# Performance work log

Measured on AMD Instinct MI355X. Metric: run time of the kernel, lower is better.

## Reference

```python
import jax, jax.numpy as jnp
import numpy as np

N = 27          # n_agents
NA = 33         # n_actions
OFF = 6         # semantic_action_offset
ATK = NA - OFF  # 27 attack actions
HID = 256       # rnn_hidden_dim
HEADS = 4
HD = 16         # head_dim
V = 8           # comm_value_dim
REL = 5
TOPK = 4
IN = 322
FLAT = HEADS * V  # 32
FUSE_SCALE = 0.1
GATE_FLOOR = 0.0
NEG = -1e10


def setup_inputs() -> dict:
    key = jax.random.key(0)
    ks = iter(jax.random.split(key, 40))
    r = lambda *s: jax.random.normal(next(ks), s, dtype=jnp.float32) * 0.05
    BS = 1024
    inp = {
        'inputs': jax.random.normal(next(ks), (BS * N, IN), dtype=jnp.float32),
        'hidden_state': jax.random.normal(next(ks), (BS * N, HID), dtype=jnp.float32),
        'relation_features': jax.random.normal(next(ks), (BS, N, N, REL), dtype=jnp.float32),
        'W1': r(HID, IN), 'b1': r(HID),
        'Wih': r(3 * HID, HID), 'bih': r(3 * HID),
        'Whh': r(3 * HID, HID), 'bhh': r(3 * HID),
        'Wp1': r(HID, HID), 'bp1': r(HID),
        'Wp2': r(NA, HID), 'bp2': r(NA),
        'Wq': r(HEADS * HD, HID), 'bq': r(HEADS * HD),
        'Wk': r(HEADS * HD, HID + REL), 'bk': r(HEADS * HD),
        'Wv': r(HEADS * V, ATK + 2), 'bv': r(HEADS * V),
        'ln_g': jnp.ones((FLAT,), jnp.float32), 'ln_b': jnp.zeros((FLAT,), jnp.float32),
        'Wg1': r(HID, HID + FLAT), 'bg1': r(HID),
        'Wg2': r(1, HID), 'bg2': jnp.full((1,), -2.5, jnp.float32),  # attack_gate_init_bias
        'Wd1': r(HID, HID + FLAT), 'bd1': r(HID),
        'Wd2': r(ATK, HID) * 0.2, 'bd2': r(ATK) * 0.2,  # small random instead of zero-init for nontrivial test
        'null_key': r(HEADS, HD), 'null_value': r(HEADS, V),
        'bs': BS,
    }
    return inp


def _topk_mask(scores, k):
    # scores: [bs, N, N+1, HEADS]; keep top-k along axis 2
    st = jnp.moveaxis(scores, 2, -1)                # [bs, N, HEADS, N+1]
    thr = jax.lax.top_k(st, k)[0][..., -1:]
    st = jnp.where(st >= thr, st, NEG)
    return jnp.moveaxis(st, -1, 2)


def _forward(inputs, hidden_state, relation_features, W1, b1, Wih, bih, Whh, bhh,
             Wp1, bp1, Wp2, bp2, Wq, bq, Wk, bk, Wv, bv, ln_g, ln_b,
             Wg1, bg1, Wg2, bg2, Wd1, bd1, Wd2, bd2, null_key, null_value, bs):
    x = jax.nn.relu(inputs @ W1.T + b1)
    h_in = hidden_state.reshape(-1, HID)
    # PyTorch GRUCell
    gi = x @ Wih.T + bih
    gh = h_in @ Whh.T + bhh
    ir, iz, inn = jnp.split(gi, 3, axis=-1)
    hr, hz, hn = jnp.split(gh, 3, axis=-1)
    rg = jax.nn.sigmoid(ir + hr)
    zg = jax.nn.sigmoid(iz + hz)
    ng = jnp.tanh(inn + rg * hn)
    h = (1.0 - zg) * ng + zg * h_in

    ah = h.reshape(bs, N, HID)                       # agent_hidden
    logits = jax.nn.relu(ah @ Wp1.T + bp1) @ Wp2.T + bp2   # [bs,N,NA]
    base_logits = logits[:, :, :OFF]
    attack_logits = logits[:, :, OFF:]

    # intent features (avail_actions=None path)
    attack_probs = jax.nn.softmax(attack_logits, axis=-1)
    top1 = jnp.max(attack_probs, axis=-1, keepdims=True)
    can_attack = jnp.ones((bs, N, 1), attack_probs.dtype)
    value_source = jnp.concatenate([attack_probs, can_attack, top1], axis=-1)
    sender_values = (value_source @ Wv.T + bv).reshape(bs, N, HEADS, V)

    queries = (ah @ Wq.T + bq).reshape(bs, N, HEADS, HD)
    # Linear over concat([sender_hidden, relation]) == split-weight sum
    Wk_h, Wk_r = Wk[:, :HID], Wk[:, HID:]
    key_h = ah @ Wk_h.T                              # [bs, N(send), A]
    key_r = jnp.einsum('bijr,ar->bija', relation_features, Wk_r)
    pair_keys = (key_h[:, None, :, :] + key_r + bk).reshape(bs, N, N, HEADS, HD)

    scale = 1.0 / np.sqrt(HD)
    scores = jnp.einsum('bihd,bijhd->bijh', queries, pair_keys) * scale
    eye = jnp.eye(N, dtype=bool)[None, :, :, None]
    scores = jnp.where(eye, NEG, scores)
    null_scores = jnp.einsum('bihd,hd->bih', queries, null_key)[:, :, None, :] * scale
    scores = jnp.concatenate([scores, null_scores], axis=2)   # [bs,N,N+1,HEADS]

    alpha = jax.nn.softmax(_topk_mask(scores, TOPK), axis=2)
    messages = (jnp.einsum('bijh,bjhv->bihv', alpha[:, :, :N], sender_values)
                + alpha[:, :, N, :, None] * null_value)        # [bs,N,HEADS,V]
    flat = messages.reshape(bs, N, FLAT)
    mu = jnp.mean(flat, axis=-1, keepdims=True)
    var = jnp.var(flat, axis=-1, keepdims=True)
    normed = (flat - mu) * jax.lax.rsqrt(var + 1e-5) * ln_g + ln_b

    fusion = jnp.concatenate([ah, normed], axis=-1)
    raw_gate = jax.nn.sigmoid(jax.nn.relu(fusion @ Wg1.T + bg1) @ Wg2.T + bg2)
    gate = GATE_FLOOR + (1.0 - GATE_FLOOR) * raw_gate
    delta = jax.nn.relu(fusion @ Wd1.T + bd1) @ Wd2.T + bd2
    fused = attack_logits + FUSE_SCALE * gate * delta
    final = jnp.concatenate([base_logits, fused], axis=-1).reshape(bs * N, NA)
    return final, h


def reference(inputs, hidden_state, relation_features, W1, b1, Wih, bih, Whh, bhh,
              Wp1, bp1, Wp2, bp2, Wq, bq, Wk, bk, Wv, bv, ln_g, ln_b,
              Wg1, bg1, Wg2, bg2, Wd1, bd1, Wd2, bd2, null_key, null_value, bs):
    return _forward(inputs, hidden_state, relation_features, W1, b1, Wih, bih, Whh, bhh,
                    Wp1, bp1, Wp2, bp2, Wq, bq, Wk, bk, Wv, bv, ln_g, ln_b,
                    Wg1, bg1, Wg2, bg2, Wd1, bd1, Wd2, bd2, null_key, null_value, bs)
```

## Files before the change

### kernel.cpp

```cpp
#include <hip/hip_runtime.h>
#include <cstdint>
#include <cstddef>

#define ROWS 27648
#define NEGV (-1e10f)

typedef __attribute__((ext_vector_type(8))) short bf16x8;
typedef __attribute__((ext_vector_type(4))) short short4v;
typedef __attribute__((ext_vector_type(4))) float f32x4;

__device__ __forceinline__ float sigmoidf_(float x) { return 1.f / (1.f + __expf(-x)); }
__device__ __forceinline__ float bf2f(short s) {
  union { float f; unsigned u; } x; x.u = ((unsigned)(unsigned short)s) << 16; return x.f;
}
__device__ __forceinline__ short f2bf(float f) {
  union { float f; unsigned u; } x; x.f = f;
  unsigned r = (x.u + 0x7fffu + ((x.u >> 16) & 1u)) >> 16;
  return (short)r;
}

#define GLDS(gp, lp) __builtin_amdgcn_global_load_lds( \
  (const __attribute__((address_space(1))) void*)(gp), \
  (__attribute__((address_space(3))) void*)(lp), 16, 0, 0)

template <int ACT, int BF16OUT>
__global__ __launch_bounds__(256) void gemm_mfma(
    const short* __restrict__ A, int lda,
    const short* __restrict__ B, int ldb,
    const float* __restrict__ bias,
    void* __restrict__ Cv, int ldc, int nstore, int K) {
  __shared__ short As[128 * 32];
  __shared__ short Bs[128 * 32];
  const int tid = threadIdx.x;
  const int wave = tid >> 6, lane = tid & 63;
  const int m0 = blockIdx.y * 128, n0 = blockIdx.x * 128;
  const int srow = lane >> 2, scol = (lane & 3) * 8;
  const int sr0 = wave * 32;
  const int wm = (wave >> 1) * 64, wn = (wave & 1) * 64;
  const int fr = lane & 15, fk = (lane >> 4) * 8;

  f32x4 acc[4][4] = {};

  const short* pA0 = A + (size_t)(m0 + sr0 + srow) * lda + scol;
  const short* pA1 = pA0 + 16 * lda;
  const short* pB0 = B + (size_t)(n0 + sr0 + srow) * ldb + scol;
  const short* pB1 = pB0 + 16 * ldb;
  short* lA0 = &As[sr0 * 32];
  short* lA1 = &As[(sr0 + 16) * 32];
  short* lB0 = &Bs[sr0 * 32];
  short* lB1 = &Bs[(sr0 + 16) * 32];

  for (int k0 = 0; k0 < K; k0 += 32) {
    GLDS(pA0 + k0, lA0);
    GLDS(pA1 + k0, lA1);
    GLDS(pB0 + k0, lB0);
    GLDS(pB1 + k0, lB1);
    __syncthreads();
    bf16x8 af[4], bfr[4];
#pragma unroll
    for (int t = 0; t < 4; ++t) {
      af[t]  = *(const bf16x8*)&As[(wm + t * 16 + fr) * 32 + fk];
      bfr[t] = *(const bf16x8*)&Bs[(wn + t * 16 + fr) * 32 + fk];
    }
#pragma unroll
    for (int i = 0; i < 4; ++i)
#pragma unroll
      for (int j = 0; j < 4; ++j)
        acc[i][j] = __builtin_amdgcn_mfma_f32_16x16x32_bf16(af[i], bfr[j], acc[i][j], 0, 0, 0);
    __syncthreads();
  }

  const int rbase = m0 + wm + (lane >> 4) * 4;
#pragma unroll
  for (int j = 0; j < 4; ++j) {
    const int col = n0 + wn + j * 16 + fr;
    if (col >= nstore) continue;
    const float bv = bias ? bias[col] : 0.f;
#pragma unroll
    for (int i = 0; i < 4; ++i)
#pragma unroll
      for (int r = 0; r < 4; ++r) {
        const int row = rbase + i * 16 + r;
        float v = acc[i][j][r] + bv;
        if (ACT) v = fmaxf(v, 0.f);
        if (BF16OUT) ((short*)Cv)[(size_t)row * ldc + col] = f2bf(v);
        else         ((float*)Cv)[(size_t)row * ldc + col] = v;
      }
  }
}

__global__ __launch_bounds__(256) void gemm_pqk(
    const short* __restrict__ A, const short* __restrict__ B,
    const float* __restrict__ bias,
    short* __restrict__ P1, float* __restrict__ QK) {
  __shared__ short As[128 * 32];
  __shared__ short Bs[128 * 32];
  const int tid = threadIdx.x;
  const int wave = tid >> 6, lane = tid & 63;
  const int m0 = blockIdx.y * 128, n0 = blockIdx.x * 128;
  const int srow = lane >> 2, scol = (lane & 3) * 8;
  const int sr0 = wave * 32;
  const int wm = (wave >> 1) * 64, wn = (wave & 1) * 64;
  const int fr = lane & 15, fk = (lane >> 4) * 8;

  f32x4 acc[4][4] = {};
  const short* pA0 = A + (size_t)(m0 + sr0 + srow) * 288 + scol;
  const short* pA1 = pA0 + 16 * 288;
  const short* pB0 = B + (size_t)(n0 + sr0 + srow) * 256 + scol;
  const short* pB1 = pB0 + 16 * 256;
  short* lA0 = &As[sr0 * 32];
  short* lA1 = &As[(sr0 + 16) * 32];
  short* lB0 = &Bs[sr0 * 32];
  short* lB1 = &Bs[(sr0 + 16) * 32];

  for (int k0 = 0; k0 < 256; k0 += 32) {
    GLDS(pA0 + k0, lA0);
    GLDS(pA1 + k0, lA1);
    GLDS(pB0 + k0, lB0);
    GLDS(pB1 + k0, lB1);
    __syncthreads();
    bf16x8 af[4], bfr[4];
#pragma unroll
    for (int t = 0; t < 4; ++t) {
      af[t]  = *(const bf16x8*)&As[(wm + t * 16 + fr) * 32 + fk];
      bfr[t] = *(const bf16x8*)&Bs[(wn + t * 16 + fr) * 32 + fk];
    }
#pragma unroll
    for (int i = 0; i < 4; ++i)
#pragma unroll
      for (int j = 0; j < 4; ++j)
        acc[i][j] = __builtin_amdgcn_mfma_f32_16x16x32_bf16(af[i], bfr[j], acc[i][j], 0, 0, 0);
    __syncthreads();
  }

  const int rbase = m0 + wm + (lane >> 4) * 4;
#pragma unroll
  for (int j = 0; j < 4; ++j) {
    const int col = n0 + wn + j * 16 + fr;
    if (col >= 384) continue;
    const float bv = bias[col];
#pragma unroll
    for (int i = 0; i < 4; ++i)
#pragma unroll
      for (int r = 0; r < 4; ++r) {
        const int row = rbase + i * 16 + r;
        float v = acc[i][j][r] + bv;
        if (col < 256) {
          P1[(size_t)row * 256 + col] = f2bf(fmaxf(v, 0.f));
        } else {
          QK[(size_t)row * 128 + (col - 256)] = v;
        }
      }
  }
}

__global__ __launch_bounds__(256) void conv_acts(
    const float* __restrict__ inputs, const float* __restrict__ hidden,
    short* __restrict__ xin, short* __restrict__ hid) {
  const int NX = ROWS * 352;
  int idx = blockIdx.x * 256 + threadIdx.x;
  if (idx < NX) {
    int row = idx / 352, c = idx - row * 352;
    xin[idx] = (c < 322) ? f2bf(inputs[row * 322 + c]) : (short)0;
  } else {
    int j = idx - NX;
    if (j < ROWS * 256) hid[j] = f2bf(hidden[j]);
  }
}

__global__ __launch_bounds__(256) void conv_w(
    const float* __restrict__ W1, const float* __restrict__ Wih,
    const float* __restrict__ Whh, const float* __restrict__ Wp1,
    const float* __restrict__ Wp2, const float* __restrict__ Wq,
    const float* __restrict__ Wk, const float* __restrict__ Wg1,
    const float* __restrict__ Wd1, const float* __restrict__ Wg2,
    const float* __restrict__ Wd2, const float* __restrict__ bp1,
    const float* __restrict__ bq, const float* __restrict__ bg1,
    const float* __restrict__ bd1, const float* __restrict__ bg2,
    const float* __restrict__ bd2,
    short* __restrict__ w1w, short* __restrict__ wihw, short* __restrict__ whhw,
    short* __restrict__ wp2w, short* __restrict__ wpqk, short* __restrict__ wgdw,
    short* __restrict__ wfw, float* __restrict__ bpqkb, float* __restrict__ bgd,
    float* __restrict__ bf2v) {
  int idx = blockIdx.x * 256 + threadIdx.x;
  if (idx < 90112) {
    int r = idx / 352, c = idx - r * 352;
    w1w[idx] = (c < 322) ? f2bf(W1[r * 322 + c]) : (short)0;
    return;
  }
  idx -= 90112;
  if (idx < 196608) { wihw[idx] = f2bf(Wih[idx]); return; }
  idx -= 196608;
  if (idx < 196608) { whhw[idx] = f2bf(Whh[idx]); return; }
  idx -= 196608;
  if (idx < 32768) {
    wp2w[idx] = (idx < 33 * 256) ? f2bf(Wp2[idx]) : (short)0;
    return;
  }
  idx -= 32768;
  if (idx < 131072) {
    int r = idx >> 8, c = idx & 255;
    short v = 0;
    if (r < 256) v = f2bf(Wp1[r * 256 + c]);
    else if (r < 320) v = f2bf(Wq[(r - 256) * 256 + c]);
    else if (r < 384) v = f2bf(Wk[(size_t)(r - 320) * 261 + c]);
    wpqk[idx] = v;
    return;
  }
  idx -= 131072;
  if (idx < 147456) {
    wgdw[idx] = (idx < 73728) ? f2bf(Wg1[idx]) : f2bf(Wd1[idx - 73728]);
    return;
  }
  idx -= 147456;
  if (idx < 65536) {
    int r = idx >> 9, c = idx & 511;
    short v = 0;
    if (r == 0 && c < 256) v = f2bf(Wg2[c]);
    else if (r >= 1 && r < 28 && c >= 256) v = f2bf(Wd2[(r - 1) * 256 + (c - 256)]);
    wfw[idx] = v;
    return;
  }
  idx -= 65536;
  if (idx < 384) {
    bpqkb[idx] = (idx < 256) ? bp1[idx] : ((idx < 320) ? bq[idx - 256] : 0.f);
    return;
  }
  idx -= 384;
  if (idx < 512) { bgd[idx] = (idx < 256) ? bg1[idx] : bd1[idx - 256]; return; }
  idx -= 512;
  if (idx < 128)
    bf2v[idx] = (idx == 0) ? bg2[0] : ((idx < 28) ? bd2[idx - 1] : 0.f);
}

__global__ __launch_bounds__(256) void gru_kernel(
    const short* __restrict__ GI, const short* __restrict__ GH,
    const float* __restrict__ Hin, float* __restrict__ H,
    short* __restrict__ FUS) {
  int idx = blockIdx.x * 256 + threadIdx.x;
  int row = idx >> 6;
  int c = (idx & 63) * 4;
  const short4v gr = *(const short4v*)(GI + (size_t)row * 768 + c);
  const short4v gz = *(const short4v*)(GI + (size_t)row * 768 + 256 + c);
  const short4v gn = *(const short4v*)(GI + (size_t)row * 768 + 512 + c);
  const short4v hr = *(const short4v*)(GH + (size_t)row * 768 + c);
  const short4v hz = *(const short4v*)(GH + (size_t)row * 768 + 256 + c);
  const short4v hn = *(const short4v*)(GH + (size_t)row * 768 + 512 + c);
  const f32x4 hi = *(const f32x4*)(Hin + (size_t)row * 256 + c);
  f32x4 o;
  short4v ob;
#pragma unroll
  for (int p = 0; p < 4; ++p) {
    float r = sigmoidf_(bf2f(gr[p]) + bf2f(hr[p]));
    float z = sigmoidf_(bf2f(gz[p]) + bf2f(hz[p]));
    float n = tanhf(bf2f(gn[p]) + r * bf2f(hn[p]));
    float h = (1.f - z) * n + z * hi[p];
    o[p] = h;
    ob[p] = f2bf(h);
  }
  *(f32x4*)(H + (size_t)row * 256 + c) = o;
  *(short4v*)(FUS + (size_t)row * 288 + c) = ob;
}

__global__ __launch_bounds__(256) void attn_sv_kernel(
    const float* __restrict__ QK, const float* __restrict__ rel,
    const float* __restrict__ Wk, const float* __restrict__ bk,
    const float* __restrict__ LOG, const float* __restrict__ Wv,
    const float* __restrict__ bv, const float* __restrict__ null_key,
    const float* __restrict__ null_value, const float* __restrict__ ln_g,
    const float* __restrict__ ln_b, short* __restrict__ FUS) {
  const int b = blockIdx.x;
  const int t = threadIdx.x;
  __shared__ float qk_s[27 * 129];
  __shared__ float rel_s[3645];
  __shared__ float lg_s[729];
  __shared__ float vs_s[27 * 29];
  __shared__ float sv_s[27 * 32];
  __shared__ float wv_s[32 * 29];
  __shared__ float wkr_s[320];
  __shared__ float bk_s[64], nk_s[64];
  __shared__ float nv_s[32], bv_s[32], lng_s[32], lnb_s[32];
  __shared__ float s_s[27 * 113];
  __shared__ float m_s[27 * 32];
  __shared__ float mu_s[27], rs_s[27];

  for (int idx = t; idx < 27 * 128; idx += 256) {
    int r = idx >> 7, c = idx & 127;
    qk_s[r * 129 + c] = QK[(size_t)(b * 27 + r) * 128 + c];
  }
  for (int idx = t; idx < 3645; idx += 256) rel_s[idx] = rel[(size_t)b * 3645 + idx];
  for (int idx = t; idx < 729; idx += 256) {
    int i = idx / 27, j = idx - i * 27;
    lg_s[idx] = LOG[(size_t)(b * 27 + i) * 33 + 6 + j];
  }
  for (int idx = t; idx < 32 * 29; idx += 256) wv_s[idx] = Wv[idx];
  if (t < 320) { int a = t / 5, r = t - a * 5; wkr_s[t] = Wk[(size_t)a * 261 + 256 + r]; }
  if (t < 64) { bk_s[t] = bk[t]; nk_s[t] = null_key[t]; }
  if (t < 32) { nv_s[t] = null_value[t]; bv_s[t] = bv[t]; lng_s[t] = ln_g[t]; lnb_s[t] = ln_b[t]; }
  __syncthreads();

  if (t < 27) {
    float m = -INFINITY;
    for (int j = 0; j < 27; ++j) m = fmaxf(m, lg_s[t * 27 + j]);
    float s = 0.f;
    for (int j = 0; j < 27; ++j) { float e = __expf(lg_s[t * 27 + j] - m); vs_s[t * 29 + j] = e; s += e; }
    float inv = 1.f / s;
    for (int j = 0; j < 27; ++j) vs_s[t * 29 + j] *= inv;
    vs_s[t * 29 + 27] = 1.f;
    vs_s[t * 29 + 28] = inv;
  }
  __syncthreads();

  for (int idx = t; idx < 864; idx += 256) {
    int j = idx >> 5, o = idx & 31;
    float acc = bv_s[o];
    const float* w = &wv_s[o * 29];
    const float* v = &vs_s[j * 29];
#pragma unroll
    for (int c = 0; c < 29; ++c) acc += w[c] * v[c];
    sv_s[idx] = acc;
  }
  for (int idx = t; idx < 3024; idx += 256) {
    int i = idx / 112, r2 = idx - i * 112;
    int j = r2 >> 2, h = r2 & 3;
    float s;
    if (j < 27) {
      const float* rp = &rel_s[(i * 27 + j) * 5];
      float r0 = rp[0], r1 = rp[1], rc = rp[2], r3 = rp[3], r4 = rp[4];
      const float* q = &qk_s[i * 129];
      const float* kh = &qk_s[j * 129 + 64 + h * 16];
      s = 0.f;
#pragma unroll
      for (int d = 0; d < 16; ++d) {
        int a = h * 16 + d;
        float kr = wkr_s[a * 5] * r0 + wkr_s[a * 5 + 1] * r1 + wkr_s[a * 5 + 2] * rc +
                   wkr_s[a * 5 + 3] * r3 + wkr_s[a * 5 + 4] * r4;
        s += q[a] * (kh[d] + kr + bk_s[a]);
      }
      s *= 0.25f;
      if (j == i) s = NEGV;
    } else {
      const float* q = &qk_s[i * 129 + h * 16];
      s = 0.f;
#pragma unroll
      for (int d = 0; d < 16; ++d) s += q[d] * nk_s[h * 16 + d];
      s *= 0.25f;
    }
    s_s[i * 113 + r2] = s;
  }
  __syncthreads();

  for (int idx = t; idx < 108; idx += 256) {
    int i = idx >> 2, h = idx & 3;
    float* sp = &s_s[i * 113 + h];
    float t0 = -INFINITY, t1 = -INFINITY, t2 = -INFINITY, t3 = -INFINITY;
    for (int j = 0; j < 28; ++j) {
      float v = sp[j * 4];
      if (v > t0)      { t3 = t2; t2 = t1; t1 = t0; t0 = v; }
      else if (v > t1) { t3 = t2; t2 = t1; t1 = v; }
      else if (v > t2) { t3 = t2; t2 = v; }
      else if (v > t3) { t3 = v; }
    }
    float sum = 0.f;
    for (int j = 0; j < 28; ++j) {
      float v = sp[j * 4];
      float e = (v >= t3) ? __expf(v - t0) : 0.f;
      sp[j * 4] = e; sum += e;
    }
    float inv = 1.f / sum;
    for (int j = 0; j < 28; ++j) sp[j * 4] *= inv;
  }
  __syncthreads();

  for (int idx = t; idx < 864; idx += 256) {
    int i = idx >> 5, o = idx & 31, h = o >> 3;
    const float* al = &s_s[i * 113 + h];
    float acc = al[27 * 4] * nv_s[o];
    for (int j = 0; j < 27; ++j) acc += al[j * 4] * sv_s[j * 32 + o];
    m_s[idx] = acc;
  }
  __syncthreads();

  if (t < 27) {
    float mu = 0.f;
    for (int k = 0; k < 32; ++k) mu += m_s[t * 32 + k];
    mu *= (1.f / 32.f);
    float var = 0.f;
    for (int k = 0; k < 32; ++k) { float d = m_s[t * 32 + k] - mu; var += d * d; }
    var *= (1.f / 32.f);
    mu_s[t] = mu; rs_s[t] = rsqrtf(var + 1e-5f);
  }
  __syncthreads();
  for (int idx = t; idx < 864; idx += 256) {
    int i = idx >> 5, o = idx & 31;
    float nv = (m_s[idx] - mu_s[i]) * rs_s[i] * lng_s[o] + lnb_s[o];
    FUS[(size_t)(b * 27 + i) * 288 + 256 + o] = f2bf(nv);
  }
}

__global__ __launch_bounds__(256) void fuse_kernel(
    const float* __restrict__ GDf, const float* __restrict__ LOG,
    float* __restrict__ out) {
  int idx = blockIdx.x * 256 + threadIdx.x;
  int row = idx / 33, c = idx - row * 33;
  float v = LOG[idx];
  if (c >= 6) {
    float gate = sigmoidf_(GDf[(size_t)row * 28]);
    v += 0.1f * gate * GDf[(size_t)row * 28 + (c - 5)];
  }
  out[idx] = v;
}

extern "C" void kernel_launch(void* const* d_in, const int* in_sizes, int n_in,
                              void* d_out, int out_size, void* d_ws, size_t ws_size,
                              hipStream_t stream) {
  const float* inputs = (const float*)d_in[0];
  const float* hidden = (const float*)d_in[1];
  const float* rel    = (const float*)d_in[2];
  const float* W1  = (const float*)d_in[3];  const float* b1  = (const float*)d_in[4];
  const float* Wih = (const float*)d_in[5];  const float* bih = (const float*)d_in[6];
  const float* Whh = (const float*)d_in[7];  const float* bhh = (const float*)d_in[8];
  const float* Wp1 = (const float*)d_in[9];  const float* bp1 = (const float*)d_in[10];
  const float* Wp2 = (const float*)d_in[11]; const float* bp2 = (const float*)d_in[12];
  const float* Wq  = (const float*)d_in[13]; const float* bq  = (const float*)d_in[14];
  const float* Wk  = (const float*)d_in[15]; const float* bk  = (const float*)d_in[16];
  const float* Wv  = (const float*)d_in[17]; const float* bv  = (const float*)d_in[18];
  const float* ln_g = (const float*)d_in[19]; const float* ln_b = (const float*)d_in[20];
  const float* Wg1 = (const float*)d_in[21]; const float* bg1 = (const float*)d_in[22];
  const float* Wg2 = (const float*)d_in[23]; const float* bg2 = (const float*)d_in[24];
  const float* Wd1 = (const float*)d_in[25]; const float* bd1 = (const float*)d_in[26];
  const float* Wd2 = (const float*)d_in[27]; const float* bd2 = (const float*)d_in[28];
  const float* null_key   = (const float*)d_in[29];
  const float* null_value = (const float*)d_in[30];

  char* wsb = (char*)d_ws;
  short* GIB = (short*)(wsb + 0);
  short* GDB = (short*)(wsb + 0);
  short* XINB = (short*)(wsb + 42467328);
  short* GHB  = (short*)(wsb + 42467328);
  float* LOG  = (float*)(wsb + 42467328);
  float* QKB  = (float*)(wsb + 42467328 + 4194304);
  float* LOGD = (float*)(wsb + 42467328 + 20971520);
  short* XB   = (short*)(wsb + 84934656);
  short* FUS  = (short*)(wsb + 84934656);
  short* HIDB = (short*)(wsb + 84934656 + 16777216);
  short* P1B  = (short*)(wsb + 84934656 + 16777216);
  char* wb = wsb + 115867648;
  short* W1W   = (short*)(wb + 0);
  short* WIHW  = (short*)(wb + 180224);
  short* WHHW  = (short*)(wb + 573440);
  short* WP2W  = (short*)(wb + 966656);
  short* WPQK  = (short*)(wb + 1032192);
  short* WGDW  = (short*)(wb + 1294336);
  short* WFW   = (short*)(wb + 1589248);
  float* BPQKb = (float*)(wb + 1720320);
  float* BGD   = (float*)(wb + 1721856);
  float* BF2   = (float*)(wb + 1723904);

  float* out = (float*)d_out;
  float* H   = out + (size_t)ROWS * 33;

  conv_acts<<<65664, 256, 0, stream>>>(inputs, hidden, XINB, HIDB);
  conv_w<<<3364, 256, 0, stream>>>(W1, Wih, Whh, Wp1, Wp2, Wq, Wk, Wg1, Wd1,
                                   Wg2, Wd2, bp1, bq, bg1, bd1, bg2, bd2,
                                   W1W, WIHW, WHHW, WP2W, WPQK, WGDW, WFW,
                                   BPQKb, BGD, BF2);
  gemm_mfma<1, 1><<<dim3(2, 216), 256, 0, stream>>>(XINB, 352, W1W, 352, b1, XB, 256, 256, 352);
  gemm_mfma<0, 1><<<dim3(6, 216), 256, 0, stream>>>(XB, 256, WIHW, 256, bih, GIB, 768, 768, 256);
  gemm_mfma<0, 1><<<dim3(6, 216), 256, 0, stream>>>(HIDB, 256, WHHW, 256, bhh, GHB, 768, 768, 256);
  gru_kernel<<<6912, 256, 0, stream>>>(GIB, GHB, hidden, H, FUS);
  gemm_pqk<<<dim3(3, 216), 256, 0, stream>>>(FUS, WPQK, BPQKb, P1B, QKB);
  gemm_mfma<0, 0><<<dim3(1, 216), 256, 0, stream>>>(P1B, 256, WP2W, 256, bp2, LOG, 33, 33, 256);
  attn_sv_kernel<<<1024, 256, 0, stream>>>(QKB, rel, Wk, bk, LOG, Wv, bv,
                                           null_key, null_value, ln_g, ln_b, FUS);
  gemm_mfma<1, 1><<<dim3(4, 216), 256, 0, stream>>>(FUS, 288, WGDW, 288, BGD, GDB, 512, 512, 288);
  gemm_mfma<0, 0><<<dim3(1, 216), 256, 0, stream>>>(GDB, 512, WFW, 512, BF2, LOGD, 28, 28, 512);
  fuse_kernel<<<3564, 256, 0, stream>>>(LOGD, LOG, out);
}
```

Baseline: 446.8 us.

## Split attention into per-row SV kernel and per-query-wave attention kernel

Replaces the single per-batch attention kernel, one block of 256 threads per batch, with two kernels. The first computes the softmaxed value projection (SV) per agent row, using wave shuffles for the reductions. The second assigns one wave per query agent across 7168 blocks. It precomputes q·Wk_rel, q·bk and q·null_key per head so the relation-key term becomes a 5-term dot product, and does the layer norm with shuffles instead of shared memory and extra barriers. The aim is more parallelism and fewer serial single-thread loops, at the cost of reloading K, SV and weights once per 4-query block and an extra global round trip for SV.

Result: no change. 445.0 us (-0.4%).

```diff
diff --git a/kernel.cpp b/kernel.cpp
--- a/kernel.cpp
+++ b/kernel.cpp
@@ -262,97 +262,123 @@
   *(short4v*)(FUS + (size_t)row * 288 + c) = ob;
 }
 
-__global__ __launch_bounds__(256) void attn_sv_kernel(
+__global__ __launch_bounds__(256) void sv_kernel(
+    const float* __restrict__ logits, const float* __restrict__ Wv,
+    const float* __restrict__ bv, float* __restrict__ SV) {
+  const int wave = threadIdx.x >> 6;
+  const int lane = threadIdx.x & 63;
+  const int row = blockIdx.x * 4 + wave;
+  __shared__ float vs_s[4][29];
+  float v = (lane < 27) ? logits[(size_t)row * 33 + 6 + lane] : -INFINITY;
+  float m = v;
+#pragma unroll
+  for (int off = 32; off; off >>= 1) m = fmaxf(m, __shfl_xor(m, off));
+  float e = (lane < 27) ? __expf(v - m) : 0.f;
+  float s = e;
+#pragma unroll
+  for (int off = 32; off; off >>= 1) s += __shfl_xor(s, off);
+  if (lane < 27) vs_s[wave][lane] = e / s;
+  if (lane == 27) vs_s[wave][27] = 1.f;
+  if (lane == 28) vs_s[wave][28] = 1.f / s;
+  __syncthreads();
+  if (lane < 32) {
+    float acc = bv[lane];
+    const float* w = Wv + lane * 29;
+#pragma unroll
+    for (int c = 0; c < 29; ++c) acc += w[c] * vs_s[wave][c];
+    SV[(size_t)row * 32 + lane] = acc;
+  }
+}
+
+__global__ __launch_bounds__(256) void attn2_kernel(
     const float* __restrict__ QK, const float* __restrict__ rel,
     const float* __restrict__ Wk, const float* __restrict__ bk,
-    const float* __restrict__ LOG, const float* __restrict__ Wv,
-    const float* __restrict__ bv, const float* __restrict__ null_key,
+    const float* __restrict__ SV, const float* __restrict__ null_key,
     const float* __restrict__ null_value, const float* __restrict__ ln_g,
     const float* __restrict__ ln_b, short* __restrict__ FUS) {
-  const int b = blockIdx.x;
+  const int b  = blockIdx.x / 7;
+  const int iq = blockIdx.x - b * 7;
   const int t = threadIdx.x;
-  __shared__ float qk_s[27 * 129];
-  __shared__ float rel_s[3645];
-  __shared__ float lg_s[729];
-  __shared__ float vs_s[27 * 29];
+  const int wave = t >> 6, lane = t & 63;
+  const int i = iq * 4 + wave;
+  const int iw = (i < 27) ? i : 26;
+
+  __shared__ float kh_s[27 * 64];
   __shared__ float sv_s[27 * 32];
-  __shared__ float wv_s[32 * 29];
+  __shared__ float q_s[4][64];
   __shared__ float wkr_s[320];
   __shared__ float bk_s[64], nk_s[64];
-  __shared__ float nv_s[32], bv_s[32], lng_s[32], lnb_s[32];
-  __shared__ float s_s[27 * 113];
-  __shared__ float m_s[27 * 32];
-  __shared__ float mu_s[27], rs_s[27];
-
-  for (int idx = t; idx < 27 * 128; idx += 256) {
-    int r = idx >> 7, c = idx & 127;
-    qk_s[r * 129 + c] = QK[(size_t)(b * 27 + r) * 128 + c];
-  }
-  for (int idx = t; idx < 3645; idx += 256) rel_s[idx] = rel[(size_t)b * 3645 + idx];
-  for (int idx = t; idx < 729; idx += 256) {
-    int i = idx / 27, j = idx - i * 27;
-    lg_s[idx] = LOG[(size_t)(b * 27 + i) * 33 + 6 + j];
-  }
-  for (int idx = t; idx < 32 * 29; idx += 256) wv_s[idx] = Wv[idx];
+  __shared__ float nv_s[32], lng_s[32], lnb_s[32];
+  __shared__ float rel_s[4][136];
+  __shared__ float qws[4][28];
+  __shared__ float s_row[4][112];
+
+  for (int idx = t; idx < 27 * 64; idx += 256) {
+    int r = idx >> 6, c = idx & 63;
+    kh_s[idx] = QK[(size_t)(b * 27 + r) * 128 + 64 + c];
+  }
+  for (int idx = t; idx < 27 * 32; idx += 256)
+    sv_s[idx] = SV[(size_t)b * 864 + idx];
+  q_s[wave][lane] = QK[(size_t)(b * 27 + iw) * 128 + lane];
   if (t < 320) { int a = t / 5, r = t - a * 5; wkr_s[t] = Wk[(size_t)a * 261 + 256 + r]; }
-  if (t < 64) { bk_s[t] = bk[t]; nk_s[t] = null_key[t]; }
-  if (t < 32) { nv_s[t] = null_value[t]; bv_s[t] = bv[t]; lng_s[t] = ln_g[t]; lnb_s[t] = ln_b[t]; }
+  if (t >= 320 && t < 384) bk_s[t - 320] = bk[t - 320];
+  if (t >= 384 && t < 448) nk_s[t - 384] = null_key[t - 384];
+  if (t >= 448 && t < 480) nv_s[t - 448] = null_value[t - 448];
+  if (t >= 480 && t < 512) { lng_s[t - 480] = ln_g[t - 480]; lnb_s[t - 480] = ln_b[t - 480]; }
+  for (int idx = lane; idx < 135; idx += 64)
+    rel_s[wave][idx] = rel[(size_t)(b * 27 + iw) * 135 + idx];
   __syncthreads();
 
-  if (t < 27) {
-    float m = -INFINITY;
-    for (int j = 0; j < 27; ++j) m = fmaxf(m, lg_s[t * 27 + j]);
-    float s = 0.f;
-    for (int j = 0; j < 27; ++j) { float e = __expf(lg_s[t * 27 + j] - m); vs_s[t * 29 + j] = e; s += e; }
-    float inv = 1.f / s;
-    for (int j = 0; j < 27; ++j) vs_s[t * 29 + j] *= inv;
-    vs_s[t * 29 + 27] = 1.f;
-    vs_s[t * 29 + 28] = inv;
+  if (lane < 28) {
+    float acc = 0.f;
+    if (lane < 20) {
+      const int h = lane / 5, r = lane - h * 5;
+#pragma unroll
+      for (int d = 0; d < 16; ++d)
+        acc += q_s[wave][h * 16 + d] * wkr_s[(h * 16 + d) * 5 + r];
+    } else if (lane < 24) {
+      const int h = lane - 20;
+#pragma unroll
+      for (int d = 0; d < 16; ++d)
+        acc += q_s[wave][h * 16 + d] * bk_s[h * 16 + d];
+    } else {
+      const int h = lane - 24;
+#pragma unroll
+      for (int d = 0; d < 16; ++d)
+        acc += q_s[wave][h * 16 + d] * nk_s[h * 16 + d];
+    }
+    qws[wave][lane] = acc;
   }
   __syncthreads();
 
-  for (int idx = t; idx < 864; idx += 256) {
-    int j = idx >> 5, o = idx & 31;
-    float acc = bv_s[o];
-    const float* w = &wv_s[o * 29];
-    const float* v = &vs_s[j * 29];
-#pragma unroll
-    for (int c = 0; c < 29; ++c) acc += w[c] * v[c];
-    sv_s[idx] = acc;
-  }
-  for (int idx = t; idx < 3024; idx += 256) {
-    int i = idx / 112, r2 = idx - i * 112;
-    int j = r2 >> 2, h = r2 & 3;
-    float s;
-    if (j < 27) {
-      const float* rp = &rel_s[(i * 27 + j) * 5];
-      float r0 = rp[0], r1 = rp[1], rc = rp[2], r3 = rp[3], r4 = rp[4];
-      const float* q = &qk_s[i * 129];
-      const float* kh = &qk_s[j * 129 + 64 + h * 16];
-      s = 0.f;
-#pragma unroll
-      for (int d = 0; d < 16; ++d) {
-        int a = h * 16 + d;
-        float kr = wkr_s[a * 5] * r0 + wkr_s[a * 5 + 1] * r1 + wkr_s[a * 5 + 2] * rc +
-                   wkr_s[a * 5 + 3] * r3 + wkr_s[a * 5 + 4] * r4;
-        s += q[a] * (kh[d] + kr + bk_s[a]);
+#pragma unroll
+  for (int pass = 0; pass < 2; ++pass) {
+    const int item = pass * 64 + lane;
+    if (item < 112) {
+      const int j = item >> 2, h = item & 3;
+      float s;
+      if (j < 27) {
+        float acc = qws[wave][20 + h];
+        const float* q  = &q_s[wave][h * 16];
+        const float* kh = &kh_s[j * 64 + h * 16];
+#pragma unroll
+        for (int d = 0; d < 16; ++d) acc += q[d] * kh[d];
+        const float* rp = &rel_s[wave][j * 5];
+        const float* qw = &qws[wave][h * 5];
+#pragma unroll
+        for (int r = 0; r < 5; ++r) acc += rp[r] * qw[r];
+        s = acc * 0.25f;
+        if (j == i) s = NEGV;
+      } else {
+        s = qws[wave][24 + h] * 0.25f;
       }
-      s *= 0.25f;
-      if (j == i) s = NEGV;
-    } else {
-      const float* q = &qk_s[i * 129 + h * 16];
-      s = 0.f;
-#pragma unroll
-      for (int d = 0; d < 16; ++d) s += q[d] * nk_s[h * 16 + d];
-      s *= 0.25f;
+      s_row[wave][item] = s;
     }
-    s_s[i * 113 + r2] = s;
   }
   __syncthreads();
 
-  for (int idx = t; idx < 108; idx += 256) {
-    int i = idx >> 2, h = idx & 3;
-    float* sp = &s_s[i * 113 + h];
+  if (lane < 4) {
+    float* sp = &s_row[wave][lane];
     float t0 = -INFINITY, t1 = -INFINITY, t2 = -INFINITY, t3 = -INFINITY;
     for (int j = 0; j < 28; ++j) {
       float v = sp[j * 4];
@@ -367,34 +393,28 @@
       float e = (v >= t3) ? __expf(v - t0) : 0.f;
       sp[j * 4] = e; sum += e;
     }
-    float inv = 1.f / sum;
+    const float inv = 1.f / sum;
     for (int j = 0; j < 28; ++j) sp[j * 4] *= inv;
   }
   __syncthreads();
 
-  for (int idx = t; idx < 864; idx += 256) {
-    int i = idx >> 5, o = idx & 31, h = o >> 3;
-    const float* al = &s_s[i * 113 + h];
-    float acc = al[27 * 4] * nv_s[o];
-    for (int j = 0; j < 27; ++j) acc += al[j * 4] * sv_s[j * 32 + o];
-    m_s[idx] = acc;
-  }
-  __syncthreads();
-
-  if (t < 27) {
-    float mu = 0.f;
-    for (int k = 0; k < 32; ++k) mu += m_s[t * 32 + k];
-    mu *= (1.f / 32.f);
-    float var = 0.f;
-    for (int k = 0; k < 32; ++k) { float d = m_s[t * 32 + k] - mu; var += d * d; }
-    var *= (1.f / 32.f);
-    mu_s[t] = mu; rs_s[t] = rsqrtf(var + 1e-5f);
-  }
-  __syncthreads();
-  for (int idx = t; idx < 864; idx += 256) {
-    int i = idx >> 5, o = idx & 31;
-    float nv = (m_s[idx] - mu_s[i]) * rs_s[i] * lng_s[o] + lnb_s[o];
-    FUS[(size_t)(b * 27 + i) * 288 + 256 + o] = f2bf(nv);
+  if (lane < 32) {
+    const int h = lane >> 3;
+    const float* al = &s_row[wave][h];
+    float acc = al[27 * 4] * nv_s[lane];
+    for (int j = 0; j < 27; ++j) acc += al[j * 4] * sv_s[j * 32 + lane];
+    float sum = acc;
+#pragma unroll
+    for (int off = 16; off; off >>= 1) sum += __shfl_xor(sum, off);
+    const float mu = sum * (1.f / 32.f);
+    float d = acc - mu;
+    float sq = d * d;
+#pragma unroll
+    for (int off = 16; off; off >>= 1) sq += __shfl_xor(sq, off);
+    const float rs = rsqrtf(sq * (1.f / 32.f) + 1e-5f);
+    const float nv = d * rs * lng_s[lane] + lnb_s[lane];
+    if (i < 27)
+      FUS[(size_t)(b * 27 + i) * 288 + 256 + lane] = f2bf(nv);
   }
 }
 
@@ -440,6 +460,7 @@
   short* GHB  = (short*)(wsb + 42467328);
   float* LOG  = (float*)(wsb + 42467328);
   float* QKB  = (float*)(wsb + 42467328 + 4194304);
+  float* SVB  = (float*)(wsb + 42467328 + 16777216);
   float* LOGD = (float*)(wsb + 42467328 + 20971520);
   short* XB   = (short*)(wsb + 84934656);
   short* FUS  = (short*)(wsb + 84934656);
@@ -471,8 +492,9 @@
   gru_kernel<<<6912, 256, 0, stream>>>(GIB, GHB, hidden, H, FUS);
   gemm_pqk<<<dim3(3, 216), 256, 0, stream>>>(FUS, WPQK, BPQKb, P1B, QKB);
   gemm_mfma<0, 0><<<dim3(1, 216), 256, 0, stream>>>(P1B, 256, WP2W, 256, bp2, LOG, 33, 33, 256);
-  attn_sv_kernel<<<1024, 256, 0, stream>>>(QKB, rel, Wk, bk, LOG, Wv, bv,
-                                           null_key, null_value, ln_g, ln_b, FUS);
+  sv_kernel<<<6912, 256, 0, stream>>>(LOG, Wv, bv, SVB);
+  attn2_kernel<<<7168, 256, 0, stream>>>(QKB, rel, Wk, bk, SVB, null_key,
+                                         null_value, ln_g, ln_b, FUS);
   gemm_mfma<1, 1><<<dim3(4, 216), 256, 0, stream>>>(FUS, 288, WGDW, 288, BGD, GDB, 512, 512, 288);
   gemm_mfma<0, 0><<<dim3(1, 216), 256, 0, stream>>>(GDB, 512, WFW, 512, BF2, LOGD, 28, 28, 512);
   fuse_kernel<<<3564, 256, 0, stream>>>(LOGD, LOG, out);
```
